# Optimization experiments

Hardware: AMD Instinct MI355X
Metric: run time of the kernel (lower is better)

The kernel has to match this reference:

```python
import jax, jax.numpy as jnp
import numpy as np
from jax import lax

IW, IH = 320, 320   # network input size (iw, ih)
K = 100             # ndet: number of detections kept


def setup_inputs() -> dict:
    key = jax.random.key(0)
    # [B, H, W, C+4]: C=80 class heatmaps + 2 (log-wh) + 2 (center offset)
    y = jax.random.normal(key, (64, 80, 80, 84), dtype=jnp.float32)
    return {"y": y}


def reference(y):
    B, H, W, Cp4 = y.shape
    C = Cp4 - 4
    scale = jnp.array([[[float(IW) / W, float(IH) / H]]], dtype=jnp.float32)  # [1,1,2]

    hm = y[..., :C]                                  # [B,H,W,C] heatmaps
    wh = jnp.exp(y[..., C:C + 2]) - 1.0              # [B,H,W,2] box sizes
    bc = y[..., C + 2:C + 4]                         # [B,H,W,2] center offsets
    wh = wh.reshape(B, H * W, 2)
    bc = bc.reshape(B, H * W, 2)

    # 3x3 max-pool NMS: keep only local peaks
    hmax = lax.reduce_window(hm, -jnp.inf, lax.max,
                             (1, 3, 3, 1), (1, 1, 1, 1), 'SAME')
    keep = hmax * (hm == hmax).astype(hm.dtype)      # [B,H,W,C]
    score = keep.reshape(B, H * W * C)

    # full descending argsort then slice top-K (faithful to tf.argsort)
    idx = jnp.argsort(-score, axis=-1)[:, :K]        # [B,K]
    k = idx % C                                      # class
    j = (idx // C) % W                               # x cell
    i = idx // (C * W)                               # y cell
    idx2d = j + i * W                                # [B,K] spatial index

    score_k = jnp.take_along_axis(score, idx, axis=1)                    # [B,K]
    centers = scale * jnp.stack((j, i), axis=-1).astype(jnp.float32) \
        + jnp.take_along_axis(bc, idx2d[..., None], axis=1)              # [B,K,2]
    wh_k = scale * jnp.take_along_axis(wh, idx2d[..., None], axis=1)     # [B,K,2]
    return (score_k, k, centers, wh_k)
```

## Files before the change

### kernel.cpp

```cpp
#include <hip/hip_runtime.h>
#include <math.h>

#define BATCH 64
#define H 80
#define W 80
#define C 80
#define CP4 84
#define TOPK 100
#define THRESH 2.5f
#define NBINS 4096
#define COLLECT_CAP 2048
#define SPLITS 2
#define RPT (H / SPLITS)
#define JT 16
#define JB (W / JT)
#define NSEG (SPLITS * JB)
#define SEGCAP 1024
#define PIX (JT + 2)
#define SLOT (PIX * 84)
#define NQ (PIX * 20)
#define BLK 320

__device__ __forceinline__ unsigned int f2key(float f) {
    unsigned int u = __float_as_uint(f);
    return (u & 0x80000000u) ? ~u : (u | 0x80000000u);
}
__device__ __forceinline__ float key2f(unsigned int k) {
    unsigned int u = (k & 0x80000000u) ? (k & 0x7FFFFFFFu) : ~k;
    return __uint_as_float(u);
}

union F4 { float4 v; float a[4]; };

__device__ __forceinline__ F4 f4max(F4 x, F4 y) {
    F4 r;
    r.a[0] = fmaxf(x.a[0], y.a[0]);
    r.a[1] = fmaxf(x.a[1], y.a[1]);
    r.a[2] = fmaxf(x.a[2], y.a[2]);
    r.a[3] = fmaxf(x.a[3], y.a[3]);
    return r;
}
__device__ __forceinline__ F4 f4neg() {
    F4 r;
    r.a[0] = r.a[1] = r.a[2] = r.a[3] = -INFINITY;
    return r;
}

__device__ __forceinline__ int slot_of(int i) { return ((i % 4) + 4) & 3; }

__device__ __forceinline__ F4 hmax_lds(const float* __restrict__ sl, int pc, F4& cen) {
    F4 l, c, r;
    l.v = *(const float4*)(sl + pc - 84);
    c.v = *(const float4*)(sl + pc);
    r.v = *(const float4*)(sl + pc + 84);
    cen = c;
    return f4max(f4max(l, r), c);
}

__global__ __launch_bounds__(BLK) void stage1_kernel(const float* __restrict__ y,
                                                     unsigned int* __restrict__ segcnt,
                                                     uint2* __restrict__ cand,
                                                     int segcap) {
    const int jb = blockIdx.x % JB;
    const int s  = (blockIdx.x / JB) % SPLITS;
    const int b  = blockIdx.x / (JB * SPLITS);
    const int t  = threadIdx.x;
    const int i0 = s * RPT;
    const int j0 = jb * JT;
    const int seg = b * NSEG + s * JB + jb;

    __shared__ float ring[4][SLOT];
    __shared__ unsigned int scount;
    if (t == 0) scount = 0u;

    const float* __restrict__ yb = y + (size_t)b * H * W * CP4;
    uint2* __restrict__ myseg = cand + (size_t)seg * segcap;

    auto stage_row = [&](int i, int sl) {
        const bool rowok = (i >= 0) && (i < H);
        #pragma unroll
        for (int q = t; q < NQ; q += BLK) {
            const int p   = q / 20;
            const int cgq = q % 20;
            const int j   = j0 - 1 + p;
            F4 v;
            if (rowok && j >= 0 && j < W)
                v.v = *(const float4*)(yb + ((size_t)i * W + j) * CP4 + cgq * 4);
            else
                v = f4neg();
            *(float4*)&ring[sl][p * 84 + cgq * 4] = v.v;
        }
    };

    const int cg = t % 20;
    const int jl = t / 20;
    const int pc = (jl + 1) * 84 + cg * 4;
    const int j  = j0 + jl;

    stage_row(i0 - 1, slot_of(i0 - 1));
    stage_row(i0,     slot_of(i0));
    stage_row(i0 + 1, slot_of(i0 + 1));
    __syncthreads();

    F4 scr, mid_c;
    F4 rm_p = hmax_lds(ring[slot_of(i0 - 1)], pc, scr);
    F4 rm_c = hmax_lds(ring[slot_of(i0)],     pc, mid_c);

    for (int i = i0; i < i0 + RPT; ++i) {
        __syncthreads();
        if (i + 2 <= i0 + RPT) stage_row(i + 2, slot_of(i + 2));

        F4 cen_n;
        const F4 rm_n = hmax_lds(ring[slot_of(i + 1)], pc, cen_n);

        const F4 m = f4max(f4max(rm_p, rm_c), rm_n);
        #pragma unroll
        for (int q = 0; q < 4; ++q) {
            const float cv = mid_c.a[q];
            if (cv > THRESH && cv == m.a[q]) {
                const unsigned int p = atomicAdd(&scount, 1u);
                if (p < (unsigned int)segcap) {
                    const unsigned int idx = (unsigned int)((i * W + j) * C + (cg * 4 + q));
                    myseg[p] = make_uint2(f2key(cv), idx);
                }
            }
        }
        rm_p = rm_c; rm_c = rm_n; mid_c = cen_n;
    }

    __syncthreads();
    if (t == 0) segcnt[seg] = min(scount, (unsigned int)segcap);
}

__global__ __launch_bounds__(256) void stage2_kernel(const float* __restrict__ y,
                                                     const unsigned int* __restrict__ segcnt,
                                                     const uint2* __restrict__ cand,
                                                     int segcap,
                                                     float* __restrict__ out) {
    const int b = blockIdx.x;
    const int t = threadIdx.x;

    __shared__ unsigned int hist[NBINS];
    __shared__ uint2 coll[COLLECT_CAP];
    __shared__ unsigned int csum[256];
    __shared__ unsigned int scnt[NSEG];
    __shared__ unsigned int sT, sM;

    if (t < NSEG) scnt[t] = min(segcnt[b * NSEG + t], (unsigned int)segcap);
    for (int q = t; q < NBINS; q += 256) hist[q] = 0u;
    if (t == 0) sM = 0u;
    __syncthreads();

    for (int sg = 0; sg < NSEG; ++sg) {
        const uint2* __restrict__ cb = cand + (size_t)(b * NSEG + sg) * segcap;
        const unsigned int n = scnt[sg];
        for (unsigned int q = t; q < n; q += 256u)
            atomicAdd(&hist[cb[q].x >> 20], 1u);
    }
    __syncthreads();

    unsigned int sacc = 0;
    #pragma unroll
    for (int q = 0; q < 16; ++q) sacc += hist[t * 16 + q];
    csum[t] = sacc;
    __syncthreads();

    if (t == 0) {
        unsigned int cum = 0;
        int T = 0;
        bool found = false;
        for (int ch = 255; ch >= 0 && !found; --ch) {
            if (cum + csum[ch] >= (unsigned int)TOPK) {
                for (int bin = ch * 16 + 15; bin >= ch * 16; --bin) {
                    cum += hist[bin];
                    if (cum >= (unsigned int)TOPK) { T = bin; found = true; break; }
                }
            } else {
                cum += csum[ch];
            }
        }
        sT = found ? (unsigned int)T : 0u;
    }
    __syncthreads();

    const unsigned int T = sT;
    for (int sg = 0; sg < NSEG; ++sg) {
        const uint2* __restrict__ cb = cand + (size_t)(b * NSEG + sg) * segcap;
        const unsigned int n = scnt[sg];
        for (unsigned int q = t; q < n; q += 256u) {
            const uint2 e = cb[q];
            if ((e.x >> 20) >= T) {
                const unsigned int p = atomicAdd(&sM, 1u);
                if (p < (unsigned int)COLLECT_CAP) coll[p] = e;
            }
        }
    }
    __syncthreads();

    const unsigned int M = min(sM, (unsigned int)COLLECT_CAP);

    for (unsigned int q = t; q < M; q += 256u) {
        const uint2 e = coll[q];
        unsigned int r = 0;
        for (unsigned int jx = 0; jx < M; ++jx) {
            const uint2 o = coll[jx];
            r += (o.x > e.x) || (o.x == e.x && o.y < e.y);
        }
        if (r < (unsigned int)TOPK) {
            const float score = key2f(e.x);
            const unsigned int idx = e.y;
            const unsigned int c  = idx % C;
            const unsigned int j2 = (idx / C) % W;
            const unsigned int i2 = idx / (C * W);
            const float* __restrict__ p = y + ((size_t)(b * H + i2) * W + j2) * CP4;
            const float w0 = expf(p[C + 0]) - 1.0f;
            const float w1 = expf(p[C + 1]) - 1.0f;
            const float b0 = p[C + 2];
            const float b1 = p[C + 3];
            const int o1 = b * TOPK + r;
            out[o1] = score;
            out[BATCH * TOPK + o1] = (float)c;
            out[2 * BATCH * TOPK + 2 * o1 + 0] = 4.0f * (float)j2 + b0;
            out[2 * BATCH * TOPK + 2 * o1 + 1] = 4.0f * (float)i2 + b1;
            out[4 * BATCH * TOPK + 2 * o1 + 0] = 4.0f * w0;
            out[4 * BATCH * TOPK + 2 * o1 + 1] = 4.0f * w1;
        }
    }

    for (unsigned int q = M + t; q < (unsigned int)TOPK; q += 256u) {
        const int o1 = b * TOPK + q;
        out[o1] = 0.0f;
        out[BATCH * TOPK + o1] = 0.0f;
        out[2 * BATCH * TOPK + 2 * o1 + 0] = 0.0f;
        out[2 * BATCH * TOPK + 2 * o1 + 1] = 0.0f;
        out[4 * BATCH * TOPK + 2 * o1 + 0] = 0.0f;
        out[4 * BATCH * TOPK + 2 * o1 + 1] = 0.0f;
    }
}

extern "C" void kernel_launch(void* const* d_in, const int* in_sizes, int n_in,
                              void* d_out, int out_size, void* d_ws, size_t ws_size,
                              hipStream_t stream) {
    const float* y = (const float*)d_in[0];
    float* out = (float*)d_out;

    unsigned int* segcnt = (unsigned int*)d_ws;
    uint2* cand = (uint2*)((char*)d_ws + 8192);

    int segcap = SEGCAP;
    const size_t avail = ws_size > 8192 ? ws_size - 8192 : 0;
    const size_t maxseg = avail / ((size_t)BATCH * NSEG * sizeof(uint2));
    if (maxseg < (size_t)segcap) segcap = (int)maxseg;

    stage1_kernel<<<BATCH * SPLITS * JB, BLK, 0, stream>>>(y, segcnt, cand, segcap);
    stage2_kernel<<<BATCH, 256, 0, stream>>>(y, segcnt, cand, segcap, out);
}
```

Before: 235.0 us.

## Replace LDS ring buffer with per-thread column streaming and lazy horizontal check

Stage 1 no longer stages rows into a shared-memory ring with per-row barriers. Each thread streams its own column of float4 values from global memory, applies the vertical 3-max first, and re-reads the horizontal neighbours from global memory only for candidates above threshold that pass the vertical test. Splits go from 2 to 4 to raise block count. This removes LDS traffic and the per-row __syncthreads, at the cost of scattered uncoalesced global loads for surviving candidates and more segments in stage 2.

Result: slower. 289.1 us (+23.1%).

```diff
diff --git a/kernel.cpp b/kernel.cpp
--- a/kernel.cpp
+++ b/kernel.cpp
@@ -10,15 +10,12 @@
 #define THRESH 2.5f
 #define NBINS 4096
 #define COLLECT_CAP 2048
-#define SPLITS 2
+#define SPLITS 4
 #define RPT (H / SPLITS)
 #define JT 16
 #define JB (W / JT)
 #define NSEG (SPLITS * JB)
 #define SEGCAP 1024
-#define PIX (JT + 2)
-#define SLOT (PIX * 84)
-#define NQ (PIX * 20)
 #define BLK 320
 
 __device__ __forceinline__ unsigned int f2key(float f) {
@@ -44,17 +41,6 @@
     F4 r;
     r.a[0] = r.a[1] = r.a[2] = r.a[3] = -INFINITY;
     return r;
-}
-
-__device__ __forceinline__ int slot_of(int i) { return ((i % 4) + 4) & 3; }
-
-__device__ __forceinline__ F4 hmax_lds(const float* __restrict__ sl, int pc, F4& cen) {
-    F4 l, c, r;
-    l.v = *(const float4*)(sl + pc - 84);
-    c.v = *(const float4*)(sl + pc);
-    r.v = *(const float4*)(sl + pc + 84);
-    cen = c;
-    return f4max(f4max(l, r), c);
 }
 
 __global__ __launch_bounds__(BLK) void stage1_kernel(const float* __restrict__ y,
@@ -65,67 +51,63 @@
     const int s  = (blockIdx.x / JB) % SPLITS;
     const int b  = blockIdx.x / (JB * SPLITS);
     const int t  = threadIdx.x;
+    const int cg = t % 20;
+    const int jl = t / 20;
+    const int j  = jb * JT + jl;
     const int i0 = s * RPT;
-    const int j0 = jb * JT;
     const int seg = b * NSEG + s * JB + jb;
-
-    __shared__ float ring[4][SLOT];
+    const int iend = i0 + RPT;
+
     __shared__ unsigned int scount;
     if (t == 0) scount = 0u;
-
-    const float* __restrict__ yb = y + (size_t)b * H * W * CP4;
+    __syncthreads();
+
+    const float* __restrict__ yb  = y + (size_t)b * H * W * CP4;
+    const float* __restrict__ col = yb + (size_t)j * CP4 + cg * 4;
     uint2* __restrict__ myseg = cand + (size_t)seg * segcap;
 
-    auto stage_row = [&](int i, int sl) {
-        const bool rowok = (i >= 0) && (i < H);
-        #pragma unroll
-        for (int q = t; q < NQ; q += BLK) {
-            const int p   = q / 20;
-            const int cgq = q % 20;
-            const int j   = j0 - 1 + p;
-            F4 v;
-            if (rowok && j >= 0 && j < W)
-                v.v = *(const float4*)(yb + ((size_t)i * W + j) * CP4 + cgq * 4);
-            else
-                v = f4neg();
-            *(float4*)&ring[sl][p * 84 + cgq * 4] = v.v;
-        }
+    auto ld = [&](int i) -> F4 {
+        F4 v;
+        if (i >= 0 && i < H) v.v = *(const float4*)(col + (size_t)i * W * CP4);
+        else                 v = f4neg();
+        return v;
     };
 
-    const int cg = t % 20;
-    const int jl = t / 20;
-    const int pc = (jl + 1) * 84 + cg * 4;
-    const int j  = j0 + jl;
-
-    stage_row(i0 - 1, slot_of(i0 - 1));
-    stage_row(i0,     slot_of(i0));
-    stage_row(i0 + 1, slot_of(i0 + 1));
-    __syncthreads();
-
-    F4 scr, mid_c;
-    F4 rm_p = hmax_lds(ring[slot_of(i0 - 1)], pc, scr);
-    F4 rm_c = hmax_lds(ring[slot_of(i0)],     pc, mid_c);
-
-    for (int i = i0; i < i0 + RPT; ++i) {
-        __syncthreads();
-        if (i + 2 <= i0 + RPT) stage_row(i + 2, slot_of(i + 2));
-
-        F4 cen_n;
-        const F4 rm_n = hmax_lds(ring[slot_of(i + 1)], pc, cen_n);
-
-        const F4 m = f4max(f4max(rm_p, rm_c), rm_n);
+    F4 v_p = ld(i0 - 1);
+    F4 v_c = ld(i0);
+    F4 v_n = ld(i0 + 1);
+
+    for (int i = i0; i < iend; ++i) {
+        const int inx = i + 2;
+        F4 v_d;
+        if (inx <= iend && inx < H) v_d = ld(inx);
+        else                        v_d = f4neg();
+
+        const F4 m = f4max(f4max(v_p, v_c), v_n);
         #pragma unroll
         for (int q = 0; q < 4; ++q) {
-            const float cv = mid_c.a[q];
+            const float cv = v_c.a[q];
             if (cv > THRESH && cv == m.a[q]) {
-                const unsigned int p = atomicAdd(&scount, 1u);
-                if (p < (unsigned int)segcap) {
-                    const unsigned int idx = (unsigned int)((i * W + j) * C + (cg * 4 + q));
-                    myseg[p] = make_uint2(f2key(cv), idx);
+                const int c = cg * 4 + q;
+                bool ok = true;
+                #pragma unroll
+                for (int di = -1; di <= 1; ++di) {
+                    const int ii = i + di;
+                    if (ii < 0 || ii >= H) continue;
+                    const float* __restrict__ rr = yb + ((size_t)ii * W) * CP4 + c;
+                    if (j > 0     && rr[(size_t)(j - 1) * CP4] > cv) ok = false;
+                    if (j < W - 1 && rr[(size_t)(j + 1) * CP4] > cv) ok = false;
+                }
+                if (ok) {
+                    const unsigned int p = atomicAdd(&scount, 1u);
+                    if (p < (unsigned int)segcap) {
+                        const unsigned int idx = (unsigned int)((i * W + j) * C + c);
+                        myseg[p] = make_uint2(f2key(cv), idx);
+                    }
                 }
             }
         }
-        rm_p = rm_c; rm_c = rm_n; mid_c = cen_n;
+        v_p = v_c; v_c = v_n; v_n = v_d;
     }
 
     __syncthreads();
```
